# Kernel optimization log

Hardware: AMD Instinct MI355X
Metric: run time of the kernel (lower is better)

The kernel has to match this reference:

```python
import jax, jax.numpy as jnp
import numpy as np

NUM_HEADS = 12

def setup_inputs() -> dict:
    key = jax.random.key(0)
    ks = jax.random.split(key, 5)
    B, S, E = 1, 4096, 768
    x = jax.random.normal(ks[0], (B, S, E), dtype=jnp.float32)
    Wqkv = jax.random.normal(ks[1], (3 * E, E), dtype=jnp.float32) * (E ** -0.5)
    bqkv = jax.random.normal(ks[2], (3 * E,), dtype=jnp.float32) * 0.02
    Wo = jax.random.normal(ks[3], (E, E), dtype=jnp.float32) * (E ** -0.5)
    bo = jax.random.normal(ks[4], (E,), dtype=jnp.float32) * 0.02
    return {"x": x, "Wqkv": Wqkv, "bqkv": bqkv, "Wo": Wo, "bo": bo, "window_size": 128}

def reference(x, Wqkv, bqkv, Wo, bo, window_size):
    B, S, E = x.shape
    H = NUM_HEADS
    hd = E // H
    # qkv projection: [B,S,3E] -> [B,S,H,3*hd] -> split
    qkv = (x @ Wqkv.T + bqkv).reshape(B, S, H, 3 * hd)
    q, k, v = jnp.split(qkv, 3, axis=-1)  # each [B,S,H,hd]
    q = q.transpose(0, 2, 1, 3)  # [B,H,S,hd]
    k = k.transpose(0, 2, 1, 3)
    v = v.transpose(0, 2, 1, 3)
    # dense scores, masked to local window |i-j| <= window_size
    scores = jnp.einsum('bhqd,bhkd->bhqk', q, k) / (hd ** 0.5)
    idx = jnp.arange(S)
    in_window = jnp.abs(idx[:, None] - idx[None, :]) <= window_size  # [S,S]
    scores = jnp.where(in_window[None, None, :, :], scores, -jnp.inf)
    attn = jax.nn.softmax(scores, axis=-1)
    out = jnp.einsum('bhqk,bhkd->bhqd', attn, v)  # [B,H,S,hd]
    out = out.transpose(0, 2, 1, 3).reshape(B, S, E)
    return out @ Wo.T + bo
```

## Files before the change

### kernel.cpp

```cpp
#include <hip/hip_runtime.h>


typedef __attribute__((ext_vector_type(8))) short short8;
typedef __attribute__((ext_vector_type(4))) short short4v;
typedef __attribute__((ext_vector_type(4))) float f32x4;

#define S_LEN 4096
#define EMB   768
#define NH    12
#define HD    64
#define QT    64
#define WMAX  128
#define NKT   20
#define VSTR  332

#if defined(__HIP_DEVICE_COMPILE__)
#define MFMA16(a, b, c) __builtin_amdgcn_mfma_f32_16x16x16bf16_1k(a, b, c, 0, 0, 0)
#else
#define MFMA16(a, b, c) (c)
#endif

__device__ __forceinline__ short f2bf(float f) {
    union { unsigned int i; float f; } c;
    c.f = f;
    unsigned int i = c.i;
    unsigned int r = (i + 0x7FFFu + ((i >> 16) & 1u)) >> 16;
    return (short)(unsigned short)r;
}

#define NX4  (S_LEN * EMB / 4)
#define NW4  (3 * EMB * EMB / 4)
#define NO4  (EMB * EMB / 4)
__global__ __launch_bounds__(256) void convert_all(
    const float* __restrict__ x, const float* __restrict__ wqkv,
    const float* __restrict__ wo, short* __restrict__ xb,
    short* __restrict__ wqkvb, short* __restrict__ wob)
{
    int i = blockIdx.x * 256 + threadIdx.x;
    const float* src; short* dst; int off;
    if (i < NX4)            { src = x;    dst = xb;    off = i; }
    else if (i < NX4 + NW4) { src = wqkv; dst = wqkvb; off = i - NX4; }
    else                    { src = wo;   dst = wob;   off = i - NX4 - NW4; }
    float4 v = ((const float4*)src)[off];
    short4v o = { f2bf(v.x), f2bf(v.y), f2bf(v.z), f2bf(v.w) };
    *(short4v*)(dst + (size_t)off * 4) = o;
}

template <int MODE>
__global__ __launch_bounds__(256) void gemm_bt_bias(
    const short* __restrict__ A, const short* __restrict__ B,
    const float* __restrict__ bias, void* __restrict__ Cv,
    int M, int N, int K)
{
    __shared__ __align__(16) short As[2][128 * 32];
    __shared__ __align__(16) short Bs[2][128 * 32];

    const int t = threadIdx.x;
    const int w = t >> 6, l = t & 63;
    const int quad = l >> 4, lane16 = l & 15;
    const int m0 = blockIdx.y * 128, n0 = blockIdx.x * 128;
    const int wm = (w >> 1) * 64, wn = (w & 1) * 64;

    f32x4 acc[4][4];
#pragma unroll
    for (int i = 0; i < 4; ++i)
#pragma unroll
        for (int j = 0; j < 4; ++j) acc[i][j] = (f32x4){0.f, 0.f, 0.f, 0.f};

    const int NKI = K >> 5;

    auto stage = [&](int ki, int b) {
#pragma unroll
        for (int i = 0; i < 2; ++i) {
            int c = i * 256 + t;
            int r = c >> 2, kc = c & 3;
#if defined(__HIP_DEVICE_COMPILE__) && __has_builtin(__builtin_amdgcn_global_load_lds)
            __builtin_amdgcn_global_load_lds(
                (const __attribute__((address_space(1))) void*)(A + (size_t)(m0 + r) * K + ki * 32 + kc * 8),
                (__attribute__((address_space(3))) void*)(As[b] + c * 8), 16, 0, 0);
            __builtin_amdgcn_global_load_lds(
                (const __attribute__((address_space(1))) void*)(B + (size_t)(n0 + r) * K + ki * 32 + kc * 8),
                (__attribute__((address_space(3))) void*)(Bs[b] + c * 8), 16, 0, 0);
#else
            *(short8*)(As[b] + c * 8) = *(const short8*)(A + (size_t)(m0 + r) * K + ki * 32 + kc * 8);
            *(short8*)(Bs[b] + c * 8) = *(const short8*)(B + (size_t)(n0 + r) * K + ki * 32 + kc * 8);
#endif
        }
    };

    stage(0, 0);
    for (int kb = 0; kb < NKI; ++kb) {
        const int cur = kb & 1;
        __syncthreads();
        if (kb + 1 < NKI) stage(kb + 1, cur ^ 1);

        short8 af[4], bfr[4];
#pragma unroll
        for (int mt = 0; mt < 4; ++mt)
            af[mt] = *(const short8*)(As[cur] + (wm + mt * 16 + lane16) * 32 + quad * 8);
#pragma unroll
        for (int nt = 0; nt < 4; ++nt)
            bfr[nt] = *(const short8*)(Bs[cur] + (wn + nt * 16 + lane16) * 32 + quad * 8);
#pragma unroll
        for (int mt = 0; mt < 4; ++mt)
#pragma unroll
            for (int nt = 0; nt < 4; ++nt)
                acc[mt][nt] = __builtin_amdgcn_mfma_f32_16x16x32_bf16(
                    af[mt], bfr[nt], acc[mt][nt], 0, 0, 0);
    }

#pragma unroll
    for (int nt = 0; nt < 4; ++nt) {
        int col = n0 + wn + nt * 16 + lane16;
        float bv = bias[col];
        int h = col / 192;
        int rem = col - h * 192;
        int ty = rem >> 6, d = rem & 63;
        short* qdst = (short*)Cv + (((size_t)ty * NH + h) * S_LEN) * HD + d;
#pragma unroll
        for (int mt = 0; mt < 4; ++mt) {
#pragma unroll
            for (int r = 0; r < 4; ++r) {
                int row = m0 + wm + mt * 16 + quad * 4 + r;
                float v = acc[mt][nt][r] + bv;
                if (MODE == 0)
                    ((short*)Cv)[(size_t)row * N + col] = f2bf(v);
                else if (MODE == 1)
                    ((float*)Cv)[(size_t)row * N + col] = v;
                else
                    qdst[(size_t)row * HD] = f2bf(v);
            }
        }
    }
}

__global__ __launch_bounds__(256, 3) void attn_win(
    const short* __restrict__ qsplit, const int* __restrict__ wptr,
    short* __restrict__ attn_out)
{
    __shared__ __align__(16) short KV[64 * VSTR];

    const int t = threadIdx.x;
    const int w = t >> 6, l = t & 63;
    const int quad = l >> 4, lane16 = l & 15;

    const int id = blockIdx.x;
    const int xcd = id & 7, j = id >> 3;
    const int h = j >> 3;
    const int q0 = ((xcd << 3) + (j & 7)) * QT;
    const int W = *wptr;
    const int kbase = q0 - WMAX;

    const short* Qh = qsplit + (size_t)h * S_LEN * HD;
    const short* Kh = qsplit + (size_t)(NH + h) * S_LEN * HD;
    const short* Vh = qsplit + (size_t)(2 * NH + h) * S_LEN * HD;

#pragma unroll
    for (int i = 0; i < 10; ++i) {
        int c = i * 256 + t;
        int r = c >> 3, gs = c & 7;
        int g = gs ^ (r & 7);
        int idx = min(max(kbase + r, 0), S_LEN - 1);
#if defined(__HIP_DEVICE_COMPILE__) && __has_builtin(__builtin_amdgcn_global_load_lds)
        __builtin_amdgcn_global_load_lds(
            (const __attribute__((address_space(1))) void*)(Kh + (size_t)idx * HD + g * 8),
            (__attribute__((address_space(3))) void*)(KV + c * 8), 16, 0, 0);
#else
        *(short8*)(KV + c * 8) = *(const short8*)(Kh + (size_t)idx * HD + g * 8);
#endif
    }
    short8 vbuf[10];
#pragma unroll
    for (int i = 0; i < 10; ++i) {
        int c = i * 256 + t;
        int kk = c >> 3, dc = c & 7;
        int idx = min(max(kbase + kk, 0), S_LEN - 1);
        vbuf[i] = *(const short8*)(Vh + (size_t)idx * HD + dc * 8);
    }
    const int qi = q0 + w * 16 + lane16;
    const short* qp = Qh + (size_t)qi * HD;
    short8 bq0 = *(const short8*)(qp + quad * 8);
    short8 bq1 = *(const short8*)(qp + 32 + quad * 8);

    __syncthreads();

    f32x4 sc[NKT];
    const int s0 = (quad ^ (lane16 & 7)) * 8;
    const int s1 = ((quad + 4) ^ (lane16 & 7)) * 8;
#pragma unroll
    for (int kt = 0; kt < NKT; ++kt) {
        const short* kp = KV + (kt * 16 + lane16) * 64;
        short8 a0 = *(const short8*)(kp + s0);
        short8 a1 = *(const short8*)(kp + s1);
        f32x4 a = (f32x4){0.f, 0.f, 0.f, 0.f};
        a = __builtin_amdgcn_mfma_f32_16x16x32_bf16(a0, bq0, a, 0, 0, 0);
        a = __builtin_amdgcn_mfma_f32_16x16x32_bf16(a1, bq1, a, 0, 0, 0);
        sc[kt] = a;
    }

    const float scale = 0.125f;
    float m = -1e30f;
#pragma unroll
    for (int kt = 0; kt < NKT; ++kt) {
#pragma unroll
        for (int r = 0; r < 4; ++r) {
            int key = kbase + kt * 16 + quad * 4 + r;
            int d = qi - key;
            int ad = d < 0 ? -d : d;
            bool valid = (key >= 0) && (key < S_LEN) && (ad <= W);
            float s = valid ? sc[kt][r] * scale : -1e30f;
            sc[kt][r] = s;
            m = fmaxf(m, s);
        }
    }
    m = fmaxf(m, __shfl_xor(m, 16, 64));
    m = fmaxf(m, __shfl_xor(m, 32, 64));

    float lsum = 0.f;
#pragma unroll
    for (int kt = 0; kt < NKT; ++kt) {
#pragma unroll
        for (int r = 0; r < 4; ++r) {
            float p = __expf(sc[kt][r] - m);
            sc[kt][r] = p;
            lsum += p;
        }
    }
    lsum += __shfl_xor(lsum, 16, 64);
    lsum += __shfl_xor(lsum, 32, 64);
    const float rl = 1.f / fmaxf(lsum, 1e-30f);

    __syncthreads();
    {
        short(*Vt)[VSTR] = (short(*)[VSTR])KV;
#pragma unroll
        for (int i = 0; i < 10; ++i) {
            int c = i * 256 + t;
            int kk = c >> 3, dc = c & 7;
#pragma unroll
            for (int jj = 0; jj < 8; ++jj)
                Vt[dc * 8 + jj][kk] = vbuf[i][jj];
        }
    }
    __syncthreads();

    short(*Vt)[VSTR] = (short(*)[VSTR])KV;
    f32x4 oacc[4];
#pragma unroll
    for (int nt = 0; nt < 4; ++nt) oacc[nt] = (f32x4){0.f, 0.f, 0.f, 0.f};

#pragma unroll
    for (int kt = 0; kt < NKT; ++kt) {
        short4v pb = { f2bf(sc[kt][0]), f2bf(sc[kt][1]),
                       f2bf(sc[kt][2]), f2bf(sc[kt][3]) };
#pragma unroll
        for (int nt = 0; nt < 4; ++nt) {
            short4v va = *(const short4v*)(&Vt[nt * 16 + lane16][kt * 16 + quad * 4]);
            oacc[nt] = MFMA16(va, pb, oacc[nt]);
        }
    }

#pragma unroll
    for (int nt = 0; nt < 4; ++nt) {
        short4v ob = { f2bf(oacc[nt][0] * rl), f2bf(oacc[nt][1] * rl),
                       f2bf(oacc[nt][2] * rl), f2bf(oacc[nt][3] * rl) };
        *(short4v*)(attn_out + (size_t)qi * EMB + h * HD + nt * 16 + quad * 4) = ob;
    }
}

extern "C" void kernel_launch(void* const* d_in, const int* in_sizes, int n_in,
                              void* d_out, int out_size, void* d_ws, size_t ws_size,
                              hipStream_t stream) {
    const float* x    = (const float*)d_in[0];
    const float* Wqkv = (const float*)d_in[1];
    const float* bqkv = (const float*)d_in[2];
    const float* Wo   = (const float*)d_in[3];
    const float* bo   = (const float*)d_in[4];
    const int*   wptr = (const int*)d_in[5];

    float* out = (float*)d_out;

    short* xb     = (short*)d_ws;
    short* wqkvb  = xb     + (size_t)S_LEN * EMB;
    short* wob    = wqkvb  + (size_t)3 * EMB * EMB;
    short* qsplit = wob    + (size_t)EMB * EMB;
    short* attn   = qsplit + (size_t)3 * NH * S_LEN * HD;

    dim3 blk(256);
    convert_all<<<dim3((NX4 + NW4 + NO4) / 256), blk, 0, stream>>>(
        x, Wqkv, Wo, xb, wqkvb, wob);
    gemm_bt_bias<2><<<dim3(2304 / 128, S_LEN / 128), blk, 0, stream>>>(
        xb, wqkvb, bqkv, qsplit, S_LEN, 2304, EMB);
    attn_win<<<dim3(S_LEN / QT * NH), blk, 0, stream>>>(qsplit, wptr, attn);
    gemm_bt_bias<1><<<dim3(EMB / 128, S_LEN / 128), blk, 0, stream>>>(
        attn, wob, bo, out, S_LEN, EMB, EMB);
}
```

Measured before the change: 150.8 us.

## Write V transposed from QKV GEMM, prescale Q, and use smaller output GEMM tiles

The QKV GEMM epilogue now writes V in a transposed [h,d,S] layout and folds the softmax scale times log2(e) into Q, so attention can load V^T into shared memory with async global-to-LDS copies instead of staging V through registers and transposing it through LDS with scalar stores. The V load is issued after the QK^T MFMAs, which lets it overlap with the softmax computation. Softmax switches to exp2f. The output projection uses a new 64x64-tile GEMM that produces more blocks for the 4096x768 problem. The cost is more rounding from scaling Q before the bf16 conversion, and a transposed V store pattern in the QKV epilogue.

```diff
diff --git a/kernel.cpp b/kernel.cpp
--- a/kernel.cpp
+++ b/kernel.cpp
@@ -12,7 +12,7 @@
 #define QT    64
 #define WMAX  128
 #define NKT   20
-#define VSTR  332
+#define QSCALE 0.18033688f
 
 #if defined(__HIP_DEVICE_COMPILE__)
 #define MFMA16(a, b, c) __builtin_amdgcn_mfma_f32_16x16x16bf16_1k(a, b, c, 0, 0, 0)
@@ -46,10 +46,9 @@
     *(short4v*)(dst + (size_t)off * 4) = o;
 }
 
-template <int MODE>
-__global__ __launch_bounds__(256) void gemm_bt_bias(
+__global__ __launch_bounds__(256) void gemm_qkv(
     const short* __restrict__ A, const short* __restrict__ B,
-    const float* __restrict__ bias, void* __restrict__ Cv,
+    const float* __restrict__ bias, short* __restrict__ Cv,
     int M, int N, int K)
 {
     __shared__ __align__(16) short As[2][128 * 32];
@@ -116,19 +115,25 @@
         int h = col / 192;
         int rem = col - h * 192;
         int ty = rem >> 6, d = rem & 63;
-        short* qdst = (short*)Cv + (((size_t)ty * NH + h) * S_LEN) * HD + d;
-#pragma unroll
-        for (int mt = 0; mt < 4; ++mt) {
-#pragma unroll
-            for (int r = 0; r < 4; ++r) {
-                int row = m0 + wm + mt * 16 + quad * 4 + r;
-                float v = acc[mt][nt][r] + bv;
-                if (MODE == 0)
-                    ((short*)Cv)[(size_t)row * N + col] = f2bf(v);
-                else if (MODE == 1)
-                    ((float*)Cv)[(size_t)row * N + col] = v;
-                else
-                    qdst[(size_t)row * HD] = f2bf(v);
+        if (ty == 2) {
+            short* vt = Cv + ((size_t)2 * NH * S_LEN) * HD + ((size_t)h * HD + d) * S_LEN;
+#pragma unroll
+            for (int mt = 0; mt < 4; ++mt) {
+                int row0 = m0 + wm + mt * 16 + quad * 4;
+                short4v o = { f2bf(acc[mt][nt][0] + bv), f2bf(acc[mt][nt][1] + bv),
+                              f2bf(acc[mt][nt][2] + bv), f2bf(acc[mt][nt][3] + bv) };
+                *(short4v*)(vt + row0) = o;
+            }
+        } else {
+            float s = (ty == 0) ? QSCALE : 1.f;
+            short* dst = Cv + ((size_t)ty * NH + h) * S_LEN * HD + d;
+#pragma unroll
+            for (int mt = 0; mt < 4; ++mt) {
+#pragma unroll
+                for (int r = 0; r < 4; ++r) {
+                    int row = m0 + wm + mt * 16 + quad * 4 + r;
+                    dst[(size_t)row * HD] = f2bf((acc[mt][nt][r] + bv) * s);
+                }
             }
         }
     }
@@ -138,7 +143,7 @@
     const short* __restrict__ qsplit, const int* __restrict__ wptr,
     short* __restrict__ attn_out)
 {
-    __shared__ __align__(16) short KV[64 * VSTR];
+    __shared__ __align__(16) short KS[320 * 64];
 
     const int t = threadIdx.x;
     const int w = t >> 6, l = t & 63;
@@ -151,9 +156,9 @@
     const int W = *wptr;
     const int kbase = q0 - WMAX;
 
-    const short* Qh = qsplit + (size_t)h * S_LEN * HD;
-    const short* Kh = qsplit + (size_t)(NH + h) * S_LEN * HD;
-    const short* Vh = qsplit + (size_t)(2 * NH + h) * S_LEN * HD;
+    const short* Qh  = qsplit + (size_t)h * S_LEN * HD;
+    const short* Kh  = qsplit + (size_t)(NH + h) * S_LEN * HD;
+    const short* VtG = qsplit + (size_t)2 * NH * S_LEN * HD + (size_t)h * HD * S_LEN;
 
 #pragma unroll
     for (int i = 0; i < 10; ++i) {
@@ -164,18 +169,10 @@
 #if defined(__HIP_DEVICE_COMPILE__) && __has_builtin(__builtin_amdgcn_global_load_lds)
         __builtin_amdgcn_global_load_lds(
             (const __attribute__((address_space(1))) void*)(Kh + (size_t)idx * HD + g * 8),
-            (__attribute__((address_space(3))) void*)(KV + c * 8), 16, 0, 0);
-#else
-        *(short8*)(KV + c * 8) = *(const short8*)(Kh + (size_t)idx * HD + g * 8);
-#endif
-    }
-    short8 vbuf[10];
-#pragma unroll
-    for (int i = 0; i < 10; ++i) {
-        int c = i * 256 + t;
-        int kk = c >> 3, dc = c & 7;
-        int idx = min(max(kbase + kk, 0), S_LEN - 1);
-        vbuf[i] = *(const short8*)(Vh + (size_t)idx * HD + dc * 8);
+            (__attribute__((address_space(3))) void*)(KS + c * 8), 16, 0, 0);
+#else
+        *(short8*)(KS + c * 8) = *(const short8*)(Kh + (size_t)idx * HD + g * 8);
+#endif
     }
     const int qi = q0 + w * 16 + lane16;
     const short* qp = Qh + (size_t)qi * HD;
@@ -185,11 +182,12 @@
     __syncthreads();
 
     f32x4 sc[NKT];
-    const int s0 = (quad ^ (lane16 & 7)) * 8;
-    const int s1 = ((quad + 4) ^ (lane16 & 7)) * 8;
+    const int d7 = lane16 & 7;
+    const int s0 = (quad ^ d7) * 8;
+    const int s1 = ((quad + 4) ^ d7) * 8;
 #pragma unroll
     for (int kt = 0; kt < NKT; ++kt) {
-        const short* kp = KV + (kt * 16 + lane16) * 64;
+        const short* kp = KS + (kt * 16 + lane16) * 64;
         short8 a0 = *(const short8*)(kp + s0);
         short8 a1 = *(const short8*)(kp + s1);
         f32x4 a = (f32x4){0.f, 0.f, 0.f, 0.f};
@@ -198,17 +196,36 @@
         sc[kt] = a;
     }
 
-    const float scale = 0.125f;
+    __syncthreads();
+
+#pragma unroll
+    for (int i = 0; i < 10; ++i) {
+        int c = i * 256 + t;
+        int d = c / 40;
+        int slot = c - d * 40;
+        int sg = slot >> 3, s = slot & 7;
+        int g = s ^ (d & 7);
+        int key0 = kbase + sg * 64 + g * 8;
+        key0 = min(max(key0, 0), S_LEN - 8);
+#if defined(__HIP_DEVICE_COMPILE__) && __has_builtin(__builtin_amdgcn_global_load_lds)
+        __builtin_amdgcn_global_load_lds(
+            (const __attribute__((address_space(1))) void*)(VtG + (size_t)d * S_LEN + key0),
+            (__attribute__((address_space(3))) void*)(KS + c * 8), 16, 0, 0);
+#else
+        *(short8*)(KS + c * 8) = *(const short8*)(VtG + (size_t)d * S_LEN + key0);
+#endif
+    }
+
     float m = -1e30f;
 #pragma unroll
     for (int kt = 0; kt < NKT; ++kt) {
 #pragma unroll
         for (int r = 0; r < 4; ++r) {
             int key = kbase + kt * 16 + quad * 4 + r;
-            int d = qi - key;
-            int ad = d < 0 ? -d : d;
-            bool valid = (key >= 0) && (key < S_LEN) && (ad <= W);
-            float s = valid ? sc[kt][r] * scale : -1e30f;
+            int dd = qi - key;
+            int ad = dd < 0 ? -dd : dd;
+            bool valid = ((unsigned)key < S_LEN) && (ad <= W);
+            float s = valid ? sc[kt][r] : -1e30f;
             sc[kt][r] = s;
             m = fmaxf(m, s);
         }
@@ -221,7 +238,7 @@
     for (int kt = 0; kt < NKT; ++kt) {
 #pragma unroll
         for (int r = 0; r < 4; ++r) {
-            float p = __expf(sc[kt][r] - m);
+            float p = exp2f(sc[kt][r] - m);
             sc[kt][r] = p;
             lsum += p;
         }
@@ -231,20 +248,7 @@
     const float rl = 1.f / fmaxf(lsum, 1e-30f);
 
     __syncthreads();
-    {
-        short(*Vt)[VSTR] = (short(*)[VSTR])KV;
-#pragma unroll
-        for (int i = 0; i < 10; ++i) {
-            int c = i * 256 + t;
-            int kk = c >> 3, dc = c & 7;
-#pragma unroll
-            for (int jj = 0; jj < 8; ++jj)
-                Vt[dc * 8 + jj][kk] = vbuf[i][jj];
-        }
-    }
-    __syncthreads();
-
-    short(*Vt)[VSTR] = (short(*)[VSTR])KV;
+
     f32x4 oacc[4];
 #pragma unroll
     for (int nt = 0; nt < 4; ++nt) oacc[nt] = (f32x4){0.f, 0.f, 0.f, 0.f};
@@ -253,9 +257,11 @@
     for (int kt = 0; kt < NKT; ++kt) {
         short4v pb = { f2bf(sc[kt][0]), f2bf(sc[kt][1]),
                        f2bf(sc[kt][2]), f2bf(sc[kt][3]) };
+        int G = kt * 2 + (quad >> 1);
+        int off = (G >> 3) * 64 + ((G & 7) ^ d7) * 8 + (quad & 1) * 4;
 #pragma unroll
         for (int nt = 0; nt < 4; ++nt) {
-            short4v va = *(const short4v*)(&Vt[nt * 16 + lane16][kt * 16 + quad * 4]);
+            short4v va = *(const short4v*)(KS + (nt * 16 + lane16) * 320 + off);
             oacc[nt] = MFMA16(va, pb, oacc[nt]);
         }
     }
@@ -265,6 +271,93 @@
         short4v ob = { f2bf(oacc[nt][0] * rl), f2bf(oacc[nt][1] * rl),
                        f2bf(oacc[nt][2] * rl), f2bf(oacc[nt][3] * rl) };
         *(short4v*)(attn_out + (size_t)qi * EMB + h * HD + nt * 16 + quad * 4) = ob;
+    }
+}
+
+__global__ __launch_bounds__(256) void gemm_out64(
+    const short* __restrict__ A, const short* __restrict__ B,
+    const float* __restrict__ bias, float* __restrict__ C,
+    int M, int N, int K)
+{
+    __shared__ __align__(16) short As[2][64 * 64];
+    __shared__ __align__(16) short Bs[2][64 * 64];
+
+    const int t = threadIdx.x;
+    const int w = t >> 6, l = t & 63;
+    const int quad = l >> 4, lane16 = l & 15;
+    const int m0 = blockIdx.y * 64, n0 = blockIdx.x * 64;
+    const int wm = (w >> 1) * 32, wn = (w & 1) * 32;
+
+    f32x4 acc[2][2];
+#pragma unroll
+    for (int i = 0; i < 2; ++i)
+#pragma unroll
+        for (int j = 0; j < 2; ++j) acc[i][j] = (f32x4){0.f, 0.f, 0.f, 0.f};
+
+    const int NKI = K >> 6;
+
+    auto stage = [&](int ki, int b) {
+#pragma unroll
+        for (int i = 0; i < 2; ++i) {
+            int c = i * 256 + t;
+            int r = c >> 3, kc = c & 7;
+            int g = kc ^ (r & 7);
+#if defined(__HIP_DEVICE_COMPILE__) && __has_builtin(__builtin_amdgcn_global_load_lds)
+            __builtin_amdgcn_global_load_lds(
+                (const __attribute__((address_space(1))) void*)(A + (size_t)(m0 + r) * K + ki * 64 + g * 8),
+                (__attribute__((address_space(3))) void*)(As[b] + c * 8), 16, 0, 0);
+            __builtin_amdgcn_global_load_lds(
+                (const __attribute__((address_space(1))) void*)(B + (size_t)(n0 + r) * K + ki * 64 + g * 8),
+                (__attribute__((address_space(3))) void*)(Bs[b] + c * 8), 16, 0, 0);
+#else
+            *(short8*)(As[b] + c * 8) = *(const short8*)(A + (size_t)(m0 + r) * K + ki * 64 + g * 8);
+            *(short8*)(Bs[b] + c * 8) = *(const short8*)(B + (size_t)(n0 + r) * K + ki * 64 + g * 8);
+#endif
+        }
+    };
+
+    stage(0, 0);
+    for (int kb = 0; kb < NKI; ++kb) {
+        const int cur = kb & 1;
+        __syncthreads();
+        if (kb + 1 < NKI) stage(kb + 1, cur ^ 1);
+
+#pragma unroll
+        for (int ks = 0; ks < 2; ++ks) {
+            short8 af[2], bfr[2];
+#pragma unroll
+            for (int mt = 0; mt < 2; ++mt) {
+                int row = wm + mt * 16 + lane16;
+                int slot = (ks * 4 + quad) ^ (row & 7);
+                af[mt] = *(const short8*)(As[cur] + row * 64 + slot * 8);
+            }
+#pragma unroll
+            for (int nt = 0; nt < 2; ++nt) {
+                int row = wn + nt * 16 + lane16;
+                int slot = (ks * 4 + quad) ^ (row & 7);
+                bfr[nt] = *(const short8*)(Bs[cur] + row * 64 + slot * 8);
+            }
+#pragma unroll
+            for (int mt = 0; mt < 2; ++mt)
+#pragma unroll
+                for (int nt = 0; nt < 2; ++nt)
+                    acc[mt][nt] = __builtin_amdgcn_mfma_f32_16x16x32_bf16(
+                        af[mt], bfr[nt], acc[mt][nt], 0, 0, 0);
+        }
+    }
+
+#pragma unroll
+    for (int nt = 0; nt < 2; ++nt) {
+        int col = n0 + wn + nt * 16 + lane16;
+        float bv = bias[col];
+#pragma unroll
+        for (int mt = 0; mt < 2; ++mt) {
+#pragma unroll
+            for (int r = 0; r < 4; ++r) {
+                int row = m0 + wm + mt * 16 + quad * 4 + r;
+                C[(size_t)row * N + col] = acc[mt][nt][r] + bv;
+            }
+        }
     }
 }
 
@@ -289,9 +382,9 @@
     dim3 blk(256);
     convert_all<<<dim3((NX4 + NW4 + NO4) / 256), blk, 0, stream>>>(
         x, Wqkv, Wo, xb, wqkvb, wob);
-    gemm_bt_bias<2><<<dim3(2304 / 128, S_LEN / 128), blk, 0, stream>>>(
+    gemm_qkv<<<dim3(2304 / 128, S_LEN / 128), blk, 0, stream>>>(
         xb, wqkvb, bqkv, qsplit, S_LEN, 2304, EMB);
     attn_win<<<dim3(S_LEN / QT * NH), blk, 0, stream>>>(qsplit, wptr, attn);
-    gemm_bt_bias<1><<<dim3(EMB / 128, S_LEN / 128), blk, 0, stream>>>(
+    gemm_out64<<<dim3(EMB / 64, S_LEN / 64), blk, 0, stream>>>(
         attn, wob, bo, out, S_LEN, EMB, EMB);
 }
```

After: 138.8 us. 1.09x faster.
